# Kernel optimization log

Measured on AMD Instinct MI355X. Metric: run time of the kernel, lower is better.

The kernel has to match this reference:

```python
import jax, jax.numpy as jnp
import numpy as np

IN_CH = 384
OUT_CH = 384
EPS = 1e-5  # torch LayerNorm default


def setup_inputs() -> dict:
    key = jax.random.key(0)
    k1, k2, k3 = jax.random.split(key, 3)
    x = jax.random.normal(k1, (32, IN_CH, 64, 64), dtype=jnp.float32)
    # LayerNorm params (torch defaults: gamma=1, beta=0; randomize slightly for a stronger test)
    ln_weight = jnp.ones((IN_CH,), jnp.float32) + 0.01 * jax.random.normal(k2, (IN_CH,), jnp.float32)
    ln_bias = jnp.zeros((IN_CH,), jnp.float32)
    # Linear params, kaiming-uniform-ish scale
    bound = 1.0 / np.sqrt(IN_CH)
    W = jax.random.uniform(k3, (OUT_CH, IN_CH), jnp.float32, -bound, bound)
    b = jnp.zeros((OUT_CH,), jnp.float32)
    return {"x": x, "ln_weight": ln_weight, "ln_bias": ln_bias, "W": W, "b": b}


def reference(x, ln_weight, ln_bias, W, b):
    # x: [B, C, H, W] -> normalize over channel dim, project C->OUT_CH, GELU, back to NCHW
    xh = jnp.transpose(x, (0, 2, 3, 1))  # [B, H, W, C]
    mu = jnp.mean(xh, axis=-1, keepdims=True)
    var = jnp.mean(jnp.square(xh - mu), axis=-1, keepdims=True)
    xn = (xh - mu) * jax.lax.rsqrt(var + EPS) * ln_weight + ln_bias
    y = jnp.einsum('bhwc,oc->bhwo', xn, W) + b
    y = jax.nn.gelu(y, approximate=False)  # torch nn.GELU default is exact erf form
    return jnp.transpose(y, (0, 3, 1, 2))  # [B, OUT_CH, H, W]
```

## Files before the change

kernel.cpp:

```cpp
#include <hip/hip_runtime.h>
#include <hip/hip_bf16.h>
#include <cmath>

typedef float f32x4 __attribute__((ext_vector_type(4)));
typedef float f32x16 __attribute__((ext_vector_type(16)));
typedef __bf16 bf16x2 __attribute__((ext_vector_type(2)));
typedef __bf16 bf16x4 __attribute__((ext_vector_type(4)));
typedef __bf16 bf16x8 __attribute__((ext_vector_type(8)));

#define C_IN 384
#define C_OUT 384
#define SPB 4096
#define NPIX 131072
#define BP 64
#define LDK 392

__global__ __launch_bounds__(128) void ppl_prep_kernel(const float* __restrict__ W,
                                                       const float* __restrict__ gamma,
                                                       const float* __restrict__ beta,
                                                       const float* __restrict__ bias,
                                                       __bf16* __restrict__ Wp,
                                                       float* __restrict__ t1,
                                                       float* __restrict__ t2) {
  const int o = blockIdx.x;
  const int t = threadIdx.x;
  const float* row = W + o * C_IN;
  float s1 = 0.f, s2 = 0.f;
  for (int c = t; c < C_IN; c += 128) {
    const float w = row[c];
    const __bf16 wq = (__bf16)(w * gamma[c]);
    Wp[o * C_IN + c] = wq;
    s1 += (float)wq;
    s2 += beta[c] * w;
  }
#pragma unroll
  for (int off = 32; off > 0; off >>= 1) {
    s1 += __shfl_down(s1, off);
    s2 += __shfl_down(s2, off);
  }
  __shared__ float red[2][2];
  if ((t & 63) == 0) { red[t >> 6][0] = s1; red[t >> 6][1] = s2; }
  __syncthreads();
  if (t == 0) {
    t1[o] = red[0][0] + red[1][0];
    t2[o] = red[0][1] + red[1][1] + bias[o];
  }
}

__device__ __forceinline__ float gelu_fast(float v) {
  const float u = 0.7978845608028654f * v * __builtin_fmaf(0.044715f * v, v, 1.0f);
  const float e = __expf(-2.0f * u);
  return v * __builtin_amdgcn_rcpf(1.0f + e);
}

__global__ __launch_bounds__(512) void ppl_stats_cast_kernel(const float* __restrict__ x,
                                                             __bf16* __restrict__ xb,
                                                             float* __restrict__ mu,
                                                             float* __restrict__ rs) {
  __shared__ float sS[8][256];
  __shared__ float sQ[8][256];
  const int tid = threadIdx.x;
  const int w = tid >> 6;
  const int lane = tid & 63;
  const int p0 = blockIdx.x * 256;
  const int b = p0 >> 12;
  const int s0 = p0 & 4095;
  const int c0 = w * 48;
  const float* xp = x + (((size_t)(b * C_IN + c0)) << 12) + s0 + 4 * lane;
  __bf16* xbp = xb + (((size_t)(b * C_IN + c0)) << 12) + s0 + 4 * lane;

  f32x4 ssv = {0.f, 0.f, 0.f, 0.f};
  f32x4 qqv = {0.f, 0.f, 0.f, 0.f};
#pragma unroll
  for (int i = 0; i < 48; i += 12) {
    f32x4 L[12];
#pragma unroll
    for (int j = 0; j < 12; ++j)
      L[j] = *reinterpret_cast<const f32x4*>(xp + ((size_t)(i + j) << 12));
#pragma unroll
    for (int j = 0; j < 12; ++j) {
      const f32x4 v = L[j];
      ssv += v;
      qqv += v * v;
      bf16x4 pk;
      pk[0] = (__bf16)v[0];
      pk[1] = (__bf16)v[1];
      pk[2] = (__bf16)v[2];
      pk[3] = (__bf16)v[3];
      *reinterpret_cast<bf16x4*>(xbp + ((size_t)(i + j) << 12)) = pk;
    }
  }
  *reinterpret_cast<f32x4*>(&sS[w][4 * lane]) = ssv;
  *reinterpret_cast<f32x4*>(&sQ[w][4 * lane]) = qqv;
  __syncthreads();
  if (tid < 256) {
    float st = 0.f, qt = 0.f;
#pragma unroll
    for (int r = 0; r < 8; ++r) {
      st += sS[r][tid];
      qt += sQ[r][tid];
    }
    const float m = st * (1.0f / C_IN);
    mu[p0 + tid] = m;
    rs[p0 + tid] = rsqrtf(qt * (1.0f / C_IN) - m * m + 1e-5f);
  }
}

__global__ __launch_bounds__(256, 3) void ppl_gemm2_kernel(const __bf16* __restrict__ xb,
                                                           const __bf16* __restrict__ Wp,
                                                           const float* __restrict__ mug,
                                                           const float* __restrict__ rsg,
                                                           const float* __restrict__ t1g,
                                                           const float* __restrict__ t2g,
                                                           float* __restrict__ out) {
  __shared__ __bf16 Xs[BP][LDK];
  __shared__ float mu_s[BP];
  __shared__ float rs_s[BP];

  const int tid = threadIdx.x;
  const int w = tid >> 6;
  const int lane = tid & 63;
  const int col = lane & 31;
  const int hi = lane >> 5;
  const int p0 = blockIdx.x * BP;
  const int b = p0 >> 12;
  const int s0 = p0 & 4095;
  const int ob = w * 96;

  if (tid < BP) {
    mu_s[tid] = mug[p0 + tid];
    rs_s[tid] = rsg[p0 + tid];
  }

  const int chg = tid >> 3;
  const int px8 = (tid & 7) * 8;
  const __bf16* xsrc = xb + (((size_t)(b * C_IN)) << 12) + s0 + px8;
#pragma unroll
  for (int i = 0; i < 6; ++i) {
    const int c = 2 * chg + 64 * i;
    const bf16x8 v0 = *reinterpret_cast<const bf16x8*>(xsrc + ((size_t)c << 12));
    const bf16x8 v1 = *reinterpret_cast<const bf16x8*>(xsrc + ((size_t)(c + 1) << 12));
#pragma unroll
    for (int r = 0; r < 8; ++r) {
      bf16x2 pr;
      pr[0] = v0[r];
      pr[1] = v1[r];
      *reinterpret_cast<bf16x2*>(&Xs[px8 + r][c]) = pr;
    }
  }
  __syncthreads();

  const __bf16* wp0 = Wp + (size_t)(ob + col) * C_IN + hi * 8;
  const __bf16* wp1 = wp0 + 32 * C_IN;
  const __bf16* wp2 = wp0 + 64 * C_IN;
  const __bf16* xs0 = &Xs[col][hi * 8];
  const __bf16* xs1 = &Xs[32 + col][hi * 8];

  f32x16 acc[2][3];
#pragma unroll
  for (int m = 0; m < 2; ++m)
#pragma unroll
    for (int n = 0; n < 3; ++n)
#pragma unroll
      for (int r = 0; r < 16; ++r) acc[m][n][r] = 0.f;

#define LOADB(dst, kk)                                     \
  {                                                        \
    dst[0] = *reinterpret_cast<const bf16x8*>(wp0 + (kk)); \
    dst[1] = *reinterpret_cast<const bf16x8*>(wp1 + (kk)); \
    dst[2] = *reinterpret_cast<const bf16x8*>(wp2 + (kk)); \
  }
#define STEP(bb, kk)                                                                    \
  {                                                                                     \
    const bf16x8 a0 = *reinterpret_cast<const bf16x8*>(xs0 + (kk));                     \
    const bf16x8 a1 = *reinterpret_cast<const bf16x8*>(xs1 + (kk));                     \
    acc[0][0] = __builtin_amdgcn_mfma_f32_32x32x16_bf16(a0, bb[0], acc[0][0], 0, 0, 0); \
    acc[0][1] = __builtin_amdgcn_mfma_f32_32x32x16_bf16(a0, bb[1], acc[0][1], 0, 0, 0); \
    acc[0][2] = __builtin_amdgcn_mfma_f32_32x32x16_bf16(a0, bb[2], acc[0][2], 0, 0, 0); \
    acc[1][0] = __builtin_amdgcn_mfma_f32_32x32x16_bf16(a1, bb[0], acc[1][0], 0, 0, 0); \
    acc[1][1] = __builtin_amdgcn_mfma_f32_32x32x16_bf16(a1, bb[1], acc[1][1], 0, 0, 0); \
    acc[1][2] = __builtin_amdgcn_mfma_f32_32x32x16_bf16(a1, bb[2], acc[1][2], 0, 0, 0); \
  }

  {
    bf16x8 bA[3], bB[3];
    LOADB(bA, 0);
#pragma unroll
    for (int it = 0; it < 12; ++it) {
      const int k = it * 32;
      LOADB(bB, k + 16);
      STEP(bA, k);
      if (it < 11) LOADB(bA, k + 32);
      STEP(bB, k + 16);
    }
  }
#undef LOADB
#undef STEP

  const float t1v[3] = {t1g[ob + col], t1g[ob + 32 + col], t1g[ob + 64 + col]};
  const float t2v[3] = {t2g[ob + col], t2g[ob + 32 + col], t2g[ob + 64 + col]};
  float* outp = out + (((size_t)(b * C_OUT + ob + col)) << 12) + s0;

#pragma unroll
  for (int nf = 0; nf < 3; ++nf) {
    float* op = outp + ((size_t)nf << 17);
#pragma unroll
    for (int m = 0; m < 2; ++m) {
#pragma unroll
      for (int qd = 0; qd < 4; ++qd) {
        const int pr = m * 32 + qd * 8 + hi * 4;
        const f32x4 mu4 = *reinterpret_cast<const f32x4*>(&mu_s[pr]);
        const f32x4 rs4 = *reinterpret_cast<const f32x4*>(&rs_s[pr]);
        f32x4 y;
#pragma unroll
        for (int r = 0; r < 4; ++r) {
          const float val = rs4[r] * (acc[m][nf][qd * 4 + r] - mu4[r] * t1v[nf]) + t2v[nf];
          y[r] = gelu_fast(val);
        }
        *reinterpret_cast<f32x4*>(op + pr) = y;
      }
    }
  }
}

__global__ __launch_bounds__(256, 3) void ppl_fused_kernel(const float* __restrict__ x,
                                                           const __bf16* __restrict__ Wp,
                                                           const float* __restrict__ t1g,
                                                           const float* __restrict__ t2g,
                                                           float* __restrict__ out) {
  __shared__ __bf16 Xs[BP][LDK];
  __shared__ float sS[4][BP];
  __shared__ float sQ[4][BP];
  __shared__ float mu_s[BP];
  __shared__ float rs_s[BP];

  const int tid = threadIdx.x;
  const int w = tid >> 6;
  const int lane = tid & 63;
  const int q = tid & 15;
  const int j = tid >> 4;
  const int col = lane & 31;
  const int hi = lane >> 5;
  const int p0 = blockIdx.x * BP;
  const int b = p0 >> 12;
  const int s0 = p0 & 4095;
  const int ob = w * 96;

  const float* xq = x + (size_t)b * (C_IN * SPB) + s0 + 4 * q;

  f32x4 LA[12], LB[12];
#pragma unroll
  for (int i = 0; i < 3; ++i)
#pragma unroll
    for (int m = 0; m < 4; ++m)
      LA[i * 4 + m] = *reinterpret_cast<const f32x4*>(xq + (size_t)(64 * i + 4 * j + m) * SPB);
#pragma unroll
  for (int i = 0; i < 3; ++i)
#pragma unroll
    for (int m = 0; m < 4; ++m)
      LB[i * 4 + m] = *reinterpret_cast<const f32x4*>(xq + (size_t)(64 * (i + 3) + 4 * j + m) * SPB);

  float ss[4] = {0.f, 0.f, 0.f, 0.f};
  float qq[4] = {0.f, 0.f, 0.f, 0.f};

#define PROCESS(L, ibase)                                                   \
  {                                                                         \
    _Pragma("unroll") for (int i = 0; i < 3; ++i) {                         \
      _Pragma("unroll") for (int r = 0; r < 4; ++r) {                       \
        const float f0 = L[i * 4 + 0][r];                                   \
        const float f1 = L[i * 4 + 1][r];                                   \
        const float f2 = L[i * 4 + 2][r];                                   \
        const float f3 = L[i * 4 + 3][r];                                   \
        ss[r] += (f0 + f1) + (f2 + f3);                                     \
        qq[r] += (f0 * f0 + f1 * f1) + (f2 * f2 + f3 * f3);                 \
        bf16x4 pk;                                                          \
        pk[0] = (__bf16)f0; pk[1] = (__bf16)f1;                             \
        pk[2] = (__bf16)f2; pk[3] = (__bf16)f3;                             \
        *reinterpret_cast<bf16x4*>(&Xs[4 * q + r][64 * ((ibase) + i) + 4 * j]) = pk; \
      }                                                                     \
    }                                                                       \
  }
  PROCESS(LA, 0)
  PROCESS(LB, 3)
#undef PROCESS

#pragma unroll
  for (int r = 0; r < 4; ++r) {
    ss[r] += __shfl_xor(ss[r], 16);
    ss[r] += __shfl_xor(ss[r], 32);
    qq[r] += __shfl_xor(qq[r], 16);
    qq[r] += __shfl_xor(qq[r], 32);
  }
  if (lane < 16) {
#pragma unroll
    for (int r = 0; r < 4; ++r) {
      sS[w][4 * lane + r] = ss[r];
      sQ[w][4 * lane + r] = qq[r];
    }
  }
  __syncthreads();
  if (tid < BP) {
    const float st = sS[0][tid] + sS[1][tid] + sS[2][tid] + sS[3][tid];
    const float qt = sQ[0][tid] + sQ[1][tid] + sQ[2][tid] + sQ[3][tid];
    const float m = st * (1.0f / C_IN);
    mu_s[tid] = m;
    rs_s[tid] = rsqrtf(qt * (1.0f / C_IN) - m * m + 1e-5f);
  }
  __syncthreads();

  const __bf16* wp0 = Wp + (size_t)(ob + col) * C_IN + hi * 8;
  const __bf16* wp1 = wp0 + 32 * C_IN;
  const __bf16* wp2 = wp0 + 64 * C_IN;
  const __bf16* xs0 = &Xs[col][hi * 8];
  const __bf16* xs1 = &Xs[32 + col][hi * 8];

  f32x16 acc[2][3];
#pragma unroll
  for (int m = 0; m < 2; ++m)
#pragma unroll
    for (int n = 0; n < 3; ++n)
#pragma unroll
      for (int r = 0; r < 16; ++r) acc[m][n][r] = 0.f;

#define LOADB(dst, kk)                                     \
  {                                                        \
    dst[0] = *reinterpret_cast<const bf16x8*>(wp0 + (kk)); \
    dst[1] = *reinterpret_cast<const bf16x8*>(wp1 + (kk)); \
    dst[2] = *reinterpret_cast<const bf16x8*>(wp2 + (kk)); \
  }
#define STEP(bb, kk)                                                                    \
  {                                                                                     \
    const bf16x8 a0 = *reinterpret_cast<const bf16x8*>(xs0 + (kk));                     \
    const bf16x8 a1 = *reinterpret_cast<const bf16x8*>(xs1 + (kk));                     \
    acc[0][0] = __builtin_amdgcn_mfma_f32_32x32x16_bf16(a0, bb[0], acc[0][0], 0, 0, 0); \
    acc[0][1] = __builtin_amdgcn_mfma_f32_32x32x16_bf16(a0, bb[1], acc[0][1], 0, 0, 0); \
    acc[0][2] = __builtin_amdgcn_mfma_f32_32x32x16_bf16(a0, bb[2], acc[0][2], 0, 0, 0); \
    acc[1][0] = __builtin_amdgcn_mfma_f32_32x32x16_bf16(a1, bb[0], acc[1][0], 0, 0, 0); \
    acc[1][1] = __builtin_amdgcn_mfma_f32_32x32x16_bf16(a1, bb[1], acc[1][1], 0, 0, 0); \
    acc[1][2] = __builtin_amdgcn_mfma_f32_32x32x16_bf16(a1, bb[2], acc[1][2], 0, 0, 0); \
  }
  {
    bf16x8 bA[3], bB[3];
    LOADB(bA, 0);
#pragma unroll
    for (int it = 0; it < 12; ++it) {
      const int k = it * 32;
      LOADB(bB, k + 16);
      STEP(bA, k);
      if (it < 11) LOADB(bA, k + 32);
      STEP(bB, k + 16);
    }
  }
#undef LOADB
#undef STEP

  const float t1v[3] = {t1g[ob + col], t1g[ob + 32 + col], t1g[ob + 64 + col]};
  const float t2v[3] = {t2g[ob + col], t2g[ob + 32 + col], t2g[ob + 64 + col]};
  float* outp = out + (((size_t)(b * C_OUT + ob + col)) << 12) + s0;
#pragma unroll
  for (int nf = 0; nf < 3; ++nf) {
    float* op = outp + ((size_t)nf << 17);
#pragma unroll
    for (int m = 0; m < 2; ++m) {
#pragma unroll
      for (int qd = 0; qd < 4; ++qd) {
        const int pr = m * 32 + qd * 8 + hi * 4;
        const f32x4 mu4 = *reinterpret_cast<const f32x4*>(&mu_s[pr]);
        const f32x4 rs4 = *reinterpret_cast<const f32x4*>(&rs_s[pr]);
        f32x4 y;
#pragma unroll
        for (int r = 0; r < 4; ++r) {
          const float val = rs4[r] * (acc[m][nf][qd * 4 + r] - mu4[r] * t1v[nf]) + t2v[nf];
          y[r] = gelu_fast(val);
        }
        *reinterpret_cast<f32x4*>(op + pr) = y;
      }
    }
  }
}

extern "C" void kernel_launch(void* const* d_in, const int* in_sizes, int n_in,
                              void* d_out, int out_size, void* d_ws, size_t ws_size,
                              hipStream_t stream) {
  const float* x = (const float*)d_in[0];
  const float* gamma = (const float*)d_in[1];
  const float* beta = (const float*)d_in[2];
  const float* W = (const float*)d_in[3];
  const float* bias = (const float*)d_in[4];
  float* out = (float*)d_out;

  __bf16* Wp = (__bf16*)d_ws;
  float* t1 = (float*)(Wp + C_OUT * C_IN);
  float* t2 = t1 + C_OUT;
  float* mu = t2 + C_OUT;
  float* rs = mu + NPIX;
  __bf16* xb = (__bf16*)(rs + NPIX);

  const size_t need = (size_t)C_OUT * C_IN * 2 + 2 * C_OUT * 4 +
                      2 * (size_t)NPIX * 4 + (size_t)NPIX * C_IN * 2;

  ppl_prep_kernel<<<C_OUT, 128, 0, stream>>>(W, gamma, beta, bias, Wp, t1, t2);

  if (ws_size >= need) {
    ppl_stats_cast_kernel<<<NPIX / 256, 512, 0, stream>>>(x, xb, mu, rs);
    ppl_gemm2_kernel<<<NPIX / BP, 256, 0, stream>>>(xb, Wp, mu, rs, t1, t2, out);
  } else {
    ppl_fused_kernel<<<NPIX / BP, 256, 0, stream>>>(x, Wp, t1, t2, out);
  }
}
```

Before: 183.8 us.

## Double-buffer K-slices of X in LDS and split output channels across blocks

Replaces the GEMM kernel, which loaded the full 64x384 X tile into LDS up front, with one that streams 32-channel K slices through a double-buffered LDS ring, overlapping global loads with MFMA work. Weights are pre-packed by the prep kernel into a tiled layout (Wt) so each lane's B fragment is a contiguous 16-byte read. Each block now covers half of the output channels, which doubles the grid, and occupancy is raised to 4 blocks per SM thanks to the smaller LDS footprint. In exchange, each X tile is read twice (once per output half), there is a barrier on every K step, and the workspace holds a second copy of the weights.

```diff
diff --git a/kernel.cpp b/kernel.cpp
--- a/kernel.cpp
+++ b/kernel.cpp
@@ -14,12 +14,14 @@
 #define NPIX 131072
 #define BP 64
 #define LDK 392
+#define ROW2 34
 
 __global__ __launch_bounds__(128) void ppl_prep_kernel(const float* __restrict__ W,
                                                        const float* __restrict__ gamma,
                                                        const float* __restrict__ beta,
                                                        const float* __restrict__ bias,
                                                        __bf16* __restrict__ Wp,
+                                                       __bf16* __restrict__ Wt,
                                                        float* __restrict__ t1,
                                                        float* __restrict__ t2) {
   const int o = blockIdx.x;
@@ -30,6 +32,7 @@
     const float w = row[c];
     const __bf16 wq = (__bf16)(w * gamma[c]);
     Wp[o * C_IN + c] = wq;
+    Wt[(((size_t)(o >> 5) * 48 + (c >> 3)) << 8) + ((o & 31) << 3) + (c & 7)] = wq;
     s1 += (float)wq;
     s2 += beta[c] * w;
   }
@@ -106,14 +109,14 @@
   }
 }
 
-__global__ __launch_bounds__(256, 3) void ppl_gemm2_kernel(const __bf16* __restrict__ xb,
-                                                           const __bf16* __restrict__ Wp,
+__global__ __launch_bounds__(256, 4) void ppl_gemm3_kernel(const __bf16* __restrict__ xb,
+                                                           const __bf16* __restrict__ Wt,
                                                            const float* __restrict__ mug,
                                                            const float* __restrict__ rsg,
                                                            const float* __restrict__ t1g,
                                                            const float* __restrict__ t2g,
                                                            float* __restrict__ out) {
-  __shared__ __bf16 Xs[BP][LDK];
+  __shared__ __bf16 Xs[2][BP * ROW2];
   __shared__ float mu_s[BP];
   __shared__ float rs_s[BP];
 
@@ -122,103 +125,107 @@
   const int lane = tid & 63;
   const int col = lane & 31;
   const int hi = lane >> 5;
-  const int p0 = blockIdx.x * BP;
+  const int wm = w >> 1;
+  const int wn = w & 1;
+  const int bid = blockIdx.x;
+  const int og = bid & 1;
+  const int pt = bid >> 1;
+  const int p0 = pt * BP;
   const int b = p0 >> 12;
   const int s0 = p0 & 4095;
-  const int ob = w * 96;
 
   if (tid < BP) {
     mu_s[tid] = mug[p0 + tid];
     rs_s[tid] = rsg[p0 + tid];
   }
 
-  const int chg = tid >> 3;
-  const int px8 = (tid & 7) * 8;
-  const __bf16* xsrc = xb + (((size_t)(b * C_IN)) << 12) + s0 + px8;
-#pragma unroll
-  for (int i = 0; i < 6; ++i) {
-    const int c = 2 * chg + 64 * i;
-    const bf16x8 v0 = *reinterpret_cast<const bf16x8*>(xsrc + ((size_t)c << 12));
-    const bf16x8 v1 = *reinterpret_cast<const bf16x8*>(xsrc + ((size_t)(c + 1) << 12));
-#pragma unroll
-    for (int r = 0; r < 8; ++r) {
-      bf16x2 pr;
-      pr[0] = v0[r];
-      pr[1] = v1[r];
-      *reinterpret_cast<bf16x2*>(&Xs[px8 + r][c]) = pr;
-    }
-  }
+  const int v = tid & 15;
+  const int c2 = tid >> 4;
+  const __bf16* xsrc = xb + (((size_t)(b * C_IN) + 2 * c2) << 12) + s0 + 4 * v;
+  __bf16* xdst = &Xs[0][0] + (4 * v) * ROW2 + 2 * c2;
+
+  const int otb = og * 6 + wn * 3;
+  const __bf16* wt0 = Wt + (((size_t)(otb + 0) * 48 + hi) << 8) + col * 8;
+  const __bf16* wt1 = Wt + (((size_t)(otb + 1) * 48 + hi) << 8) + col * 8;
+  const __bf16* wt2 = Wt + (((size_t)(otb + 2) * 48 + hi) << 8) + col * 8;
+
+  const __bf16* abase = &Xs[0][0] + (wm * 32 + col) * ROW2 + hi * 8;
+
+  f32x16 acc[3];
+#pragma unroll
+  for (int n = 0; n < 3; ++n)
+#pragma unroll
+    for (int r = 0; r < 16; ++r) acc[n][r] = 0.f;
+
+  bf16x4 sA, sB;
+#define SLOAD(K)                                                    \
+  {                                                                 \
+    const __bf16* sp_ = xsrc + ((size_t)(K) << 12);                 \
+    sA = *reinterpret_cast<const bf16x4*>(sp_);                     \
+    sB = *reinterpret_cast<const bf16x4*>(sp_ + SPB);               \
+  }
+#define SWRITE(bi)                                                  \
+  {                                                                 \
+    __bf16* d_ = xdst + (bi) * (BP * ROW2);                         \
+    _Pragma("unroll") for (int r_ = 0; r_ < 4; ++r_) {              \
+      bf16x2 pr_;                                                   \
+      pr_[0] = sA[r_];                                              \
+      pr_[1] = sB[r_];                                              \
+      *reinterpret_cast<bf16x2*>(d_ + r_ * ROW2) = pr_;             \
+    }                                                               \
+  }
+
+  SLOAD(0);
+  SWRITE(0);
   __syncthreads();
 
-  const __bf16* wp0 = Wp + (size_t)(ob + col) * C_IN + hi * 8;
-  const __bf16* wp1 = wp0 + 32 * C_IN;
-  const __bf16* wp2 = wp0 + 64 * C_IN;
-  const __bf16* xs0 = &Xs[col][hi * 8];
-  const __bf16* xs1 = &Xs[32 + col][hi * 8];
-
-  f32x16 acc[2][3];
-#pragma unroll
-  for (int m = 0; m < 2; ++m)
-#pragma unroll
-    for (int n = 0; n < 3; ++n)
-#pragma unroll
-      for (int r = 0; r < 16; ++r) acc[m][n][r] = 0.f;
-
-#define LOADB(dst, kk)                                     \
-  {                                                        \
-    dst[0] = *reinterpret_cast<const bf16x8*>(wp0 + (kk)); \
-    dst[1] = *reinterpret_cast<const bf16x8*>(wp1 + (kk)); \
-    dst[2] = *reinterpret_cast<const bf16x8*>(wp2 + (kk)); \
-  }
-#define STEP(bb, kk)                                                                    \
-  {                                                                                     \
-    const bf16x8 a0 = *reinterpret_cast<const bf16x8*>(xs0 + (kk));                     \
-    const bf16x8 a1 = *reinterpret_cast<const bf16x8*>(xs1 + (kk));                     \
-    acc[0][0] = __builtin_amdgcn_mfma_f32_32x32x16_bf16(a0, bb[0], acc[0][0], 0, 0, 0); \
-    acc[0][1] = __builtin_amdgcn_mfma_f32_32x32x16_bf16(a0, bb[1], acc[0][1], 0, 0, 0); \
-    acc[0][2] = __builtin_amdgcn_mfma_f32_32x32x16_bf16(a0, bb[2], acc[0][2], 0, 0, 0); \
-    acc[1][0] = __builtin_amdgcn_mfma_f32_32x32x16_bf16(a1, bb[0], acc[1][0], 0, 0, 0); \
-    acc[1][1] = __builtin_amdgcn_mfma_f32_32x32x16_bf16(a1, bb[1], acc[1][1], 0, 0, 0); \
-    acc[1][2] = __builtin_amdgcn_mfma_f32_32x32x16_bf16(a1, bb[2], acc[1][2], 0, 0, 0); \
-  }
-
-  {
-    bf16x8 bA[3], bB[3];
-    LOADB(bA, 0);
-#pragma unroll
-    for (int it = 0; it < 12; ++it) {
-      const int k = it * 32;
-      LOADB(bB, k + 16);
-      STEP(bA, k);
-      if (it < 11) LOADB(bA, k + 32);
-      STEP(bB, k + 16);
-    }
-  }
-#undef LOADB
-#undef STEP
-
-  const float t1v[3] = {t1g[ob + col], t1g[ob + 32 + col], t1g[ob + 64 + col]};
-  const float t2v[3] = {t2g[ob + col], t2g[ob + 32 + col], t2g[ob + 64 + col]};
-  float* outp = out + (((size_t)(b * C_OUT + ob + col)) << 12) + s0;
-
-#pragma unroll
-  for (int nf = 0; nf < 3; ++nf) {
-    float* op = outp + ((size_t)nf << 17);
-#pragma unroll
-    for (int m = 0; m < 2; ++m) {
-#pragma unroll
-      for (int qd = 0; qd < 4; ++qd) {
-        const int pr = m * 32 + qd * 8 + hi * 4;
-        const f32x4 mu4 = *reinterpret_cast<const f32x4*>(&mu_s[pr]);
-        const f32x4 rs4 = *reinterpret_cast<const f32x4*>(&rs_s[pr]);
-        f32x4 y;
-#pragma unroll
-        for (int r = 0; r < 4; ++r) {
-          const float val = rs4[r] * (acc[m][nf][qd * 4 + r] - mu4[r] * t1v[nf]) + t2v[nf];
-          y[r] = gelu_fast(val);
-        }
-        *reinterpret_cast<f32x4*>(op + pr) = y;
+#pragma unroll 2
+  for (int it = 0; it < 12; ++it) {
+    if (it < 11) SLOAD(32 * (it + 1));
+
+    const __bf16* ap = abase + (it & 1) * (BP * ROW2);
+    const bf16x8 a0 = *reinterpret_cast<const bf16x8*>(ap);
+    const bf16x8 a1 = *reinterpret_cast<const bf16x8*>(ap + 16);
+
+    const int kofs = it * 1024;
+    const bf16x8 b00 = *reinterpret_cast<const bf16x8*>(wt0 + kofs);
+    const bf16x8 b01 = *reinterpret_cast<const bf16x8*>(wt1 + kofs);
+    const bf16x8 b02 = *reinterpret_cast<const bf16x8*>(wt2 + kofs);
+    const bf16x8 b10 = *reinterpret_cast<const bf16x8*>(wt0 + kofs + 512);
+    const bf16x8 b11 = *reinterpret_cast<const bf16x8*>(wt1 + kofs + 512);
+    const bf16x8 b12 = *reinterpret_cast<const bf16x8*>(wt2 + kofs + 512);
+
+    acc[0] = __builtin_amdgcn_mfma_f32_32x32x16_bf16(a0, b00, acc[0], 0, 0, 0);
+    acc[1] = __builtin_amdgcn_mfma_f32_32x32x16_bf16(a0, b01, acc[1], 0, 0, 0);
+    acc[2] = __builtin_amdgcn_mfma_f32_32x32x16_bf16(a0, b02, acc[2], 0, 0, 0);
+    acc[0] = __builtin_amdgcn_mfma_f32_32x32x16_bf16(a1, b10, acc[0], 0, 0, 0);
+    acc[1] = __builtin_amdgcn_mfma_f32_32x32x16_bf16(a1, b11, acc[1], 0, 0, 0);
+    acc[2] = __builtin_amdgcn_mfma_f32_32x32x16_bf16(a1, b12, acc[2], 0, 0, 0);
+
+    if (it < 11) SWRITE((it + 1) & 1);
+    __syncthreads();
+  }
+#undef SLOAD
+#undef SWRITE
+
+#pragma unroll
+  for (int n = 0; n < 3; ++n) {
+    const int o = og * 192 + wn * 96 + n * 32 + col;
+    const float t1v = t1g[o];
+    const float t2v = t2g[o];
+    float* op = out + (((size_t)(b * C_OUT + o)) << 12) + s0 + wm * 32;
+#pragma unroll
+    for (int qd = 0; qd < 4; ++qd) {
+      const int pr = qd * 8 + hi * 4;
+      const f32x4 mu4 = *reinterpret_cast<const f32x4*>(&mu_s[wm * 32 + pr]);
+      const f32x4 rs4 = *reinterpret_cast<const f32x4*>(&rs_s[wm * 32 + pr]);
+      f32x4 y;
+#pragma unroll
+      for (int r = 0; r < 4; ++r) {
+        const float val = rs4[r] * (acc[n][qd * 4 + r] - mu4[r] * t1v) + t2v;
+        y[r] = gelu_fast(val);
       }
+      *reinterpret_cast<f32x4*>(op + pr) = y;
     }
   }
 }
@@ -390,20 +397,21 @@
   float* out = (float*)d_out;
 
   __bf16* Wp = (__bf16*)d_ws;
-  float* t1 = (float*)(Wp + C_OUT * C_IN);
+  __bf16* Wt = Wp + C_OUT * C_IN;
+  float* t1 = (float*)(Wt + C_OUT * C_IN);
   float* t2 = t1 + C_OUT;
   float* mu = t2 + C_OUT;
   float* rs = mu + NPIX;
   __bf16* xb = (__bf16*)(rs + NPIX);
 
-  const size_t need = (size_t)C_OUT * C_IN * 2 + 2 * C_OUT * 4 +
+  const size_t need = 2 * (size_t)C_OUT * C_IN * 2 + 2 * C_OUT * 4 +
                       2 * (size_t)NPIX * 4 + (size_t)NPIX * C_IN * 2;
 
-  ppl_prep_kernel<<<C_OUT, 128, 0, stream>>>(W, gamma, beta, bias, Wp, t1, t2);
+  ppl_prep_kernel<<<C_OUT, 128, 0, stream>>>(W, gamma, beta, bias, Wp, Wt, t1, t2);
 
   if (ws_size >= need) {
     ppl_stats_cast_kernel<<<NPIX / 256, 512, 0, stream>>>(x, xb, mu, rs);
-    ppl_gemm2_kernel<<<NPIX / BP, 256, 0, stream>>>(xb, Wp, mu, rs, t1, t2, out);
+    ppl_gemm3_kernel<<<(NPIX / BP) * 2, 256, 0, stream>>>(xb, Wt, mu, rs, t1, t2, out);
   } else {
     ppl_fused_kernel<<<NPIX / BP, 256, 0, stream>>>(x, Wp, t1, t2, out);
   }
```

New measurement: 175.8 us. -4.4%, faster.
